# Performance work log

Hardware: AMD Instinct MI355X
Metric: run time of the kernel (lower is better)

The kernel has to match this reference:

```python
import jax, jax.numpy as jnp
import numpy as np

B, N, T, E, H, R = 8, 64, 128, 128, 8, 4
DH = E // H


def setup_inputs() -> dict:
    key = jax.random.key(0)
    ks = jax.random.split(key, 14)
    s = 1.0 / np.sqrt(E)
    return {
        "node_memory": jax.random.normal(ks[0], (B, N, T, E), jnp.float32),
        "subgraph_memory": jax.random.normal(ks[1], (B, N, T, E, R - 1), jnp.float32),
        "Wq": jax.random.normal(ks[2], (E, E), jnp.float32) * s,
        "bq": jnp.zeros((E,), jnp.float32),
        "Wk": jax.random.normal(ks[3], (E, E), jnp.float32) * s,
        "bk": jnp.zeros((E,), jnp.float32),
        "Wv": jax.random.normal(ks[4], (E, E), jnp.float32) * s,
        "bv": jnp.zeros((E,), jnp.float32),
        "in_w": jax.random.normal(ks[5], (3 * E, E), jnp.float32) * s,
        "in_b": jnp.zeros((3 * E,), jnp.float32),
        "out_w": jax.random.normal(ks[6], (E, E), jnp.float32) * s,
        "out_b": jnp.zeros((E,), jnp.float32),
        "fc_w": jax.random.normal(ks[7], (E, R * E), jnp.float32) * (1.0 / np.sqrt(R * E)),
        "fc_b": jnp.zeros((E,), jnp.float32),
    }


def reference(node_memory, subgraph_memory, Wq, bq, Wk, bk, Wv, bv,
              in_w, in_b, out_w, out_b, fc_w, fc_b):
    # combined: [B,N,T,R,E] = concat(node[...,None,:], subgraph permuted)
    combined = jnp.concatenate(
        [node_memory[..., None, :], jnp.swapaxes(subgraph_memory, -1, -2)], axis=-2)
    # outer QKV projections
    Q = jnp.einsum("bntrf,ef->bntre", combined, Wq) + bq
    K = jnp.einsum("bntrf,ef->bntre", combined, Wk) + bk
    V = jnp.einsum("bntrf,ef->bntre", combined, Wv) + bv
    # nn.MultiheadAttention in-projection
    q = jnp.einsum("bntre,fe->bntrf", Q, in_w[:E]) + in_b[:E]
    k = jnp.einsum("bntre,fe->bntrf", K, in_w[E:2 * E]) + in_b[E:2 * E]
    v = jnp.einsum("bntre,fe->bntrf", V, in_w[2 * E:]) + in_b[2 * E:]
    # split heads: [B,N,T,R,H,DH]
    q = q.reshape(B, N, T, R, H, DH) * (1.0 / np.sqrt(DH))
    k = k.reshape(B, N, T, R, H, DH)
    v = v.reshape(B, N, T, R, H, DH)
    scores = jnp.einsum("bntrhd,bntshd->bnthrs", q, k)  # [B,N,T,H,R,R]
    attn = jax.nn.softmax(scores, axis=-1)
    o = jnp.einsum("bnthrs,bntshd->bntrhd", attn, v).reshape(B, N, T, R, E)
    o = jnp.einsum("bntre,fe->bntrf", o, out_w) + out_b
    # concat the R representations and fuse
    o = o.reshape(B, N, T, R * E)
    return jnp.einsum("bntc,ec->bnte", o, fc_w) + fc_b
```

## Files before the change

kernel.cpp:

```cpp
#include <hip/hip_runtime.h>
#include <hip/hip_bf16.h>

constexpr int cE  = 128;
constexpr int cR  = 4;
constexpr int cNT = 65536;

typedef short s8v  __attribute__((ext_vector_type(8)));
typedef float f4v  __attribute__((ext_vector_type(4)));

static __device__ __forceinline__ unsigned short f2bf(float x) {
    union { float f; unsigned int u; } v; v.f = x;
    unsigned int r = v.u + 0x7fffu + ((v.u >> 16) & 1u);
    return (unsigned short)(r >> 16);
}

#define QB(x, C) __int_as_float(__builtin_amdgcn_update_dpp( \
            0, __float_as_int(x), C, 0xF, 0xF, false))

__global__ __launch_bounds__(256) void k_prep(
    const float* __restrict__ Wq, const float* __restrict__ Wk, const float* __restrict__ Wv,
    const float* __restrict__ in_w, const float* __restrict__ out_w, const float* __restrict__ fc_w,
    const float* __restrict__ bq, const float* __restrict__ bk, const float* __restrict__ bv,
    const float* __restrict__ in_b, const float* __restrict__ out_b, const float* __restrict__ fc_b,
    unsigned short* __restrict__ wqkv, unsigned short* __restrict__ meff,
    float* __restrict__ bqkv, float* __restrict__ beff)
{
    int bid = blockIdx.x;
    if (bid < 1792) {
        int gt = bid * 256 + (int)threadIdx.x;
        int o  = gt >> 2;
        int p  = gt & 3;
        float s;
        if (o < 3 * cE * cE) {
            int w   = o >> 14;
            int rem = o & (cE * cE - 1);
            int f = rem >> 7, g = rem & 127;
            const float* Wsel = (w == 0) ? Wq : ((w == 1) ? Wk : Wv);
            const float* iw = in_w + (size_t)(w * cE + f) * cE + p * 32;
            const float* wp = Wsel + (size_t)(p * 32) * cE + g;
            float s0 = 0.f, s1 = 0.f;
            #pragma unroll
            for (int e = 0; e < 32; e += 2) {
                s0 += iw[e]     * wp[(size_t)e * cE];
                s1 += iw[e + 1] * wp[(size_t)(e + 1) * cE];
            }
            s = s0 + s1;
            s += __shfl_xor(s, 1);
            s += __shfl_xor(s, 2);
            if (w == 0) s *= 0.25f;
            if (p == 0) wqkv[o] = f2bf(s);
        } else {
            int i2 = o - 3 * cE * cE;
            int e1 = i2 >> 9;
            int c  = i2 & 511;
            const float* fw = fc_w + (size_t)e1 * 512 + (c >> 7) * cE + p * 32;
            int ee = c & 127;
            const float* ow = out_w + (size_t)(p * 32) * cE + ee;
            float s0 = 0.f, s1 = 0.f;
            #pragma unroll
            for (int ff = 0; ff < 32; ff += 2) {
                s0 += fw[ff]     * ow[(size_t)ff * cE];
                s1 += fw[ff + 1] * ow[(size_t)(ff + 1) * cE];
            }
            s = s0 + s1;
            s += __shfl_xor(s, 1);
            s += __shfl_xor(s, 2);
            if (p == 0) meff[i2] = f2bf(s);
        }
    } else {
        int idx = (bid - 1792) * 256 + (int)threadIdx.x;
        if (idx < 384) {
            int w = idx >> 7, f = idx & 127;
            const float* bsel = (w == 0) ? bq : ((w == 1) ? bk : bv);
            const float* iw = in_w + (size_t)(w * cE + f) * cE;
            float s = 0.f;
            for (int e = 0; e < cE; ++e) s += iw[e] * bsel[e];
            s += in_b[w * cE + f];
            if (w == 0) s *= 0.25f;
            bqkv[idx] = s;
        } else {
            int f = idx - 384;
            float s = 0.f;
            for (int c = 0; c < 512; ++c) s += fc_w[(size_t)f * 512 + c] * out_b[c & 127];
            beff[f] = s + fc_b[f];
        }
    }
}

#define TOKB   32
#define TOKC   8
#define PITCH  136
#define OPITCH 520

__global__ __launch_bounds__(256) void k_main(
    const float* __restrict__ node, const float* __restrict__ sub,
    const unsigned short* __restrict__ wqkv,
    const unsigned short* __restrict__ meff,
    const float* __restrict__ bqkv,
    const float* __restrict__ beff,
    float* __restrict__ out)
{
    __shared__ unsigned short uAO[32 * PITCH];

    const int tid  = threadIdx.x;
    const int lane = tid & 63;
    const int wv   = tid >> 6;
    const int l15  = lane & 15;
    const int lq   = lane >> 4;
    const int ct0  = wv * 2;

    const int tokBlock = blockIdx.x * TOKB;

    for (int chunk = 0; chunk < TOKB / TOKC; ++chunk) {
        const int tokBase = tokBlock + chunk * TOKC;
        __syncthreads();

        {
            int tok = tid >> 5;
            int e4  = (tid & 31) * 4;
            float4 v = *(const float4*)(node + (size_t)(tokBase + tok) * cE + e4);
            *(ushort4*)&uAO[(tok * cR) * PITCH + e4] =
                make_ushort4(f2bf(v.x), f2bf(v.y), f2bf(v.z), f2bf(v.w));
        }
        {
            int tok = tid >> 5;
            int eg  = tid & 31;
            const float* sp = sub + (size_t)(tokBase + tok) * 384 + eg * 12;
            float4 f0 = *(const float4*)(sp + 0);
            float4 f1 = *(const float4*)(sp + 4);
            float4 f2 = *(const float4*)(sp + 8);
            int e0 = eg * 4;
            *(ushort4*)&uAO[(tok * cR + 1) * PITCH + e0] =
                make_ushort4(f2bf(f0.x), f2bf(f0.w), f2bf(f1.z), f2bf(f2.y));
            *(ushort4*)&uAO[(tok * cR + 2) * PITCH + e0] =
                make_ushort4(f2bf(f0.y), f2bf(f1.x), f2bf(f1.w), f2bf(f2.z));
            *(ushort4*)&uAO[(tok * cR + 3) * PITCH + e0] =
                make_ushort4(f2bf(f0.z), f2bf(f1.y), f2bf(f2.x), f2bf(f2.w));
        }
        __syncthreads();

        f4v qa[2][2], ka[2][2], va[2][2];
        #pragma unroll
        for (int rt = 0; rt < 2; ++rt)
            #pragma unroll
            for (int cc = 0; cc < 2; ++cc) {
                qa[rt][cc] = (f4v){0.f, 0.f, 0.f, 0.f};
                ka[rt][cc] = (f4v){0.f, 0.f, 0.f, 0.f};
                va[rt][cc] = (f4v){0.f, 0.f, 0.f, 0.f};
            }
        #pragma unroll
        for (int kc = 0; kc < 4; ++kc) {
            const int koff = kc * 32 + lq * 8;
            s8v a0 = *(const s8v*)&uAO[l15 * PITCH + koff];
            s8v a1 = *(const s8v*)&uAO[(16 + l15) * PITCH + koff];
            #pragma unroll
            for (int cc = 0; cc < 2; ++cc) {
                const size_t fo = (size_t)((ct0 + cc) * 16 + l15) * cE + koff;
                s8v wq_ = *(const s8v*)(wqkv + fo);
                s8v wk_ = *(const s8v*)(wqkv + 16384 + fo);
                s8v wv_ = *(const s8v*)(wqkv + 32768 + fo);
                qa[0][cc] = __builtin_amdgcn_mfma_f32_16x16x32_bf16(wq_, a0, qa[0][cc], 0, 0, 0);
                qa[1][cc] = __builtin_amdgcn_mfma_f32_16x16x32_bf16(wq_, a1, qa[1][cc], 0, 0, 0);
                ka[0][cc] = __builtin_amdgcn_mfma_f32_16x16x32_bf16(wk_, a0, ka[0][cc], 0, 0, 0);
                ka[1][cc] = __builtin_amdgcn_mfma_f32_16x16x32_bf16(wk_, a1, ka[1][cc], 0, 0, 0);
                va[0][cc] = __builtin_amdgcn_mfma_f32_16x16x32_bf16(wv_, a0, va[0][cc], 0, 0, 0);
                va[1][cc] = __builtin_amdgcn_mfma_f32_16x16x32_bf16(wv_, a1, va[1][cc], 0, 0, 0);
            }
        }
        #pragma unroll
        for (int cc = 0; cc < 2; ++cc) {
            const int fb = (ct0 + cc) * 16 + lq * 4;
            float4 b0 = *(const float4*)(bqkv + fb);
            float4 b1 = *(const float4*)(bqkv + cE + fb);
            float4 b2 = *(const float4*)(bqkv + 2 * cE + fb);
            #pragma unroll
            for (int rt = 0; rt < 2; ++rt) {
                qa[rt][cc][0] += b0.x; qa[rt][cc][1] += b0.y;
                qa[rt][cc][2] += b0.z; qa[rt][cc][3] += b0.w;
                ka[rt][cc][0] += b1.x; ka[rt][cc][1] += b1.y;
                ka[rt][cc][2] += b1.z; ka[rt][cc][3] += b1.w;
                va[rt][cc][0] += b2.x; va[rt][cc][1] += b2.y;
                va[rt][cc][2] += b2.z; va[rt][cc][3] += b2.w;
            }
        }

        __syncthreads();

        {
            const int r  = l15 & 3;
            const int tq = l15 >> 2;
            #pragma unroll
            for (int rt = 0; rt < 2; ++rt) {
                #pragma unroll
                for (int cc = 0; cc < 2; ++cc) {
                    f4v q = qa[rt][cc], k = ka[rt][cc], v = va[rt][cc];
                    float s0 = QB(k[0],0x00)*q[0] + QB(k[1],0x00)*q[1]
                             + QB(k[2],0x00)*q[2] + QB(k[3],0x00)*q[3];
                    float s1 = QB(k[0],0x55)*q[0] + QB(k[1],0x55)*q[1]
                             + QB(k[2],0x55)*q[2] + QB(k[3],0x55)*q[3];
                    float s2 = QB(k[0],0xAA)*q[0] + QB(k[1],0xAA)*q[1]
                             + QB(k[2],0xAA)*q[2] + QB(k[3],0xAA)*q[3];
                    float s3 = QB(k[0],0xFF)*q[0] + QB(k[1],0xFF)*q[1]
                             + QB(k[2],0xFF)*q[2] + QB(k[3],0xFF)*q[3];
                    s0 += __shfl_xor(s0, 16); s0 += __shfl_xor(s0, 32);
                    s1 += __shfl_xor(s1, 16); s1 += __shfl_xor(s1, 32);
                    s2 += __shfl_xor(s2, 16); s2 += __shfl_xor(s2, 32);
                    s3 += __shfl_xor(s3, 16); s3 += __shfl_xor(s3, 32);
                    float m = fmaxf(fmaxf(s0, s1), fmaxf(s2, s3));
                    float p0 = __expf(s0 - m), p1 = __expf(s1 - m);
                    float p2 = __expf(s2 - m), p3 = __expf(s3 - m);
                    float inv = 1.f / (p0 + p1 + p2 + p3);
                    p0 *= inv; p1 *= inv; p2 *= inv; p3 *= inv;
                    float o0 = p0*QB(v[0],0x00) + p1*QB(v[0],0x55)
                             + p2*QB(v[0],0xAA) + p3*QB(v[0],0xFF);
                    float o1 = p0*QB(v[1],0x00) + p1*QB(v[1],0x55)
                             + p2*QB(v[1],0xAA) + p3*QB(v[1],0xFF);
                    float o2 = p0*QB(v[2],0x00) + p1*QB(v[2],0x55)
                             + p2*QB(v[2],0xAA) + p3*QB(v[2],0xFF);
                    float o3 = p0*QB(v[3],0x00) + p1*QB(v[3],0x55)
                             + p2*QB(v[3],0xAA) + p3*QB(v[3],0xFF);
                    int tok = rt * 4 + tq;
                    *(ushort4*)&uAO[tok * OPITCH + r * cE + (ct0 + cc) * 16 + lq * 4] =
                        make_ushort4(f2bf(o0), f2bf(o1), f2bf(o2), f2bf(o3));
                }
            }
        }
        __syncthreads();

        {
            f4v acc[2];
            acc[0] = (f4v){0.f, 0.f, 0.f, 0.f};
            acc[1] = (f4v){0.f, 0.f, 0.f, 0.f};
            int arow = l15 & 7;
            #pragma unroll 4
            for (int kc = 0; kc < 16; ++kc) {
                int koff = kc * 32 + lq * 8;
                s8v a = *(const s8v*)&uAO[arow * OPITCH + koff];
                #pragma unroll
                for (int c = 0; c < 2; ++c) {
                    int e1 = (ct0 + c) * 16 + l15;
                    s8v b = *(const s8v*)(meff + (size_t)e1 * 512 + koff);
                    acc[c] = __builtin_amdgcn_mfma_f32_16x16x32_bf16(b, a, acc[c], 0, 0, 0);
                }
            }
            if (l15 < 8) {
                size_t tokOff = (size_t)(tokBase + l15) * cE;
                #pragma unroll
                for (int c = 0; c < 2; ++c) {
                    int col = (ct0 + c) * 16 + lq * 4;
                    float4 b4 = *(const float4*)&beff[col];
                    *(float4*)&out[tokOff + col] =
                        make_float4(acc[c][0] + b4.x, acc[c][1] + b4.y,
                                    acc[c][2] + b4.z, acc[c][3] + b4.w);
                }
            }
        }
    }
}

extern "C" void kernel_launch(void* const* d_in, const int* in_sizes, int n_in,
                              void* d_out, int out_size, void* d_ws, size_t ws_size,
                              hipStream_t stream) {
    const float* node  = (const float*)d_in[0];
    const float* sub   = (const float*)d_in[1];
    const float* Wq    = (const float*)d_in[2];
    const float* bq    = (const float*)d_in[3];
    const float* Wk    = (const float*)d_in[4];
    const float* bk    = (const float*)d_in[5];
    const float* Wv    = (const float*)d_in[6];
    const float* bv    = (const float*)d_in[7];
    const float* in_w  = (const float*)d_in[8];
    const float* in_b  = (const float*)d_in[9];
    const float* out_w = (const float*)d_in[10];
    const float* out_b = (const float*)d_in[11];
    const float* fc_w  = (const float*)d_in[12];
    const float* fc_b  = (const float*)d_in[13];

    unsigned short* ws_wqkv = (unsigned short*)d_ws;
    unsigned short* ws_meff = ws_wqkv + 3 * cE * cE;
    float* ws_bqkv = (float*)((char*)d_ws + (size_t)(3 * cE * cE + cE * cR * cE) * 2);
    float* ws_beff = ws_bqkv + 3 * cE;

    k_prep<<<dim3(1794), dim3(256), 0, stream>>>(Wq, Wk, Wv, in_w, out_w, fc_w,
                                                 bq, bk, bv, in_b, out_b, fc_b,
                                                 ws_wqkv, ws_meff, ws_bqkv, ws_beff);
    k_main<<<dim3(cNT / TOKB), dim3(256), 0, stream>>>(node, sub, ws_wqkv, ws_meff,
                                                       ws_bqkv, ws_beff, (float*)d_out);
}
```

Measured before the change: 348.6 us.

## Double-buffer shared tiles and prefetch next chunk's inputs into registers

Splits the single shared buffer into double-buffered input (sA) and attention-output (sO) tiles. The global loads for the next 8-token chunk are issued into registers before the QKV MFMAs of the current chunk, then converted and written to the other buffer after the attention step. This removes two of the per-chunk barriers and overlaps global memory latency with compute. It also adds a waves_per_eu(4) occupancy hint; the larger shared footprint and extra live registers may lower occupancy.

```diff
diff --git a/kernel.cpp b/kernel.cpp
--- a/kernel.cpp
+++ b/kernel.cpp
@@ -92,7 +92,8 @@
 #define PITCH  136
 #define OPITCH 520
 
-__global__ __launch_bounds__(256) void k_main(
+__global__ __launch_bounds__(256) __attribute__((amdgpu_waves_per_eu(4)))
+void k_main(
     const float* __restrict__ node, const float* __restrict__ sub,
     const unsigned short* __restrict__ wqkv,
     const unsigned short* __restrict__ meff,
@@ -100,7 +101,8 @@
     const float* __restrict__ beff,
     float* __restrict__ out)
 {
-    __shared__ unsigned short uAO[32 * PITCH];
+    __shared__ unsigned short sA[2][32 * PITCH];
+    __shared__ unsigned short sO[2][8 * OPITCH];
 
     const int tid  = threadIdx.x;
     const int lane = tid & 63;
@@ -110,34 +112,41 @@
     const int ct0  = wv * 2;
 
     const int tokBlock = blockIdx.x * TOKB;
+    const int stok = tid >> 5;
+    const int seg  = tid & 31;
+    const int e0   = seg * 4;
+
+    {
+        const float* np = node + (size_t)(tokBlock + stok) * cE + e0;
+        const float* sp = sub  + (size_t)(tokBlock + stok) * 384 + seg * 12;
+        float4 vn = *(const float4*)np;
+        float4 f0 = *(const float4*)(sp + 0);
+        float4 f1 = *(const float4*)(sp + 4);
+        float4 f2 = *(const float4*)(sp + 8);
+        *(ushort4*)&sA[0][(stok * cR) * PITCH + e0] =
+            make_ushort4(f2bf(vn.x), f2bf(vn.y), f2bf(vn.z), f2bf(vn.w));
+        *(ushort4*)&sA[0][(stok * cR + 1) * PITCH + e0] =
+            make_ushort4(f2bf(f0.x), f2bf(f0.w), f2bf(f1.z), f2bf(f2.y));
+        *(ushort4*)&sA[0][(stok * cR + 2) * PITCH + e0] =
+            make_ushort4(f2bf(f0.y), f2bf(f1.x), f2bf(f1.w), f2bf(f2.z));
+        *(ushort4*)&sA[0][(stok * cR + 3) * PITCH + e0] =
+            make_ushort4(f2bf(f0.z), f2bf(f1.y), f2bf(f2.x), f2bf(f2.w));
+    }
+    __syncthreads();
 
     for (int chunk = 0; chunk < TOKB / TOKC; ++chunk) {
+        const int cur = chunk & 1;
         const int tokBase = tokBlock + chunk * TOKC;
-        __syncthreads();
-
-        {
-            int tok = tid >> 5;
-            int e4  = (tid & 31) * 4;
-            float4 v = *(const float4*)(node + (size_t)(tokBase + tok) * cE + e4);
-            *(ushort4*)&uAO[(tok * cR) * PITCH + e4] =
-                make_ushort4(f2bf(v.x), f2bf(v.y), f2bf(v.z), f2bf(v.w));
-        }
-        {
-            int tok = tid >> 5;
-            int eg  = tid & 31;
-            const float* sp = sub + (size_t)(tokBase + tok) * 384 + eg * 12;
-            float4 f0 = *(const float4*)(sp + 0);
-            float4 f1 = *(const float4*)(sp + 4);
-            float4 f2 = *(const float4*)(sp + 8);
-            int e0 = eg * 4;
-            *(ushort4*)&uAO[(tok * cR + 1) * PITCH + e0] =
-                make_ushort4(f2bf(f0.x), f2bf(f0.w), f2bf(f1.z), f2bf(f2.y));
-            *(ushort4*)&uAO[(tok * cR + 2) * PITCH + e0] =
-                make_ushort4(f2bf(f0.y), f2bf(f1.x), f2bf(f1.w), f2bf(f2.z));
-            *(ushort4*)&uAO[(tok * cR + 3) * PITCH + e0] =
-                make_ushort4(f2bf(f0.z), f2bf(f1.y), f2bf(f2.x), f2bf(f2.w));
-        }
-        __syncthreads();
+
+        float4 vn, f0, f1, f2;
+        if (chunk < 3) {
+            const float* np = node + (size_t)(tokBase + TOKC + stok) * cE + e0;
+            const float* sp = sub  + (size_t)(tokBase + TOKC + stok) * 384 + seg * 12;
+            vn = *(const float4*)np;
+            f0 = *(const float4*)(sp + 0);
+            f1 = *(const float4*)(sp + 4);
+            f2 = *(const float4*)(sp + 8);
+        }
 
         f4v qa[2][2], ka[2][2], va[2][2];
         #pragma unroll
@@ -151,8 +160,8 @@
         #pragma unroll
         for (int kc = 0; kc < 4; ++kc) {
             const int koff = kc * 32 + lq * 8;
-            s8v a0 = *(const s8v*)&uAO[l15 * PITCH + koff];
-            s8v a1 = *(const s8v*)&uAO[(16 + l15) * PITCH + koff];
+            s8v a0 = *(const s8v*)&sA[cur][l15 * PITCH + koff];
+            s8v a1 = *(const s8v*)&sA[cur][(16 + l15) * PITCH + koff];
             #pragma unroll
             for (int cc = 0; cc < 2; ++cc) {
                 const size_t fo = (size_t)((ct0 + cc) * 16 + l15) * cE + koff;
@@ -183,8 +192,6 @@
                 va[rt][cc][2] += b2.z; va[rt][cc][3] += b2.w;
             }
         }
-
-        __syncthreads();
 
         {
             const int r  = l15 & 3;
@@ -220,11 +227,24 @@
                     float o3 = p0*QB(v[3],0x00) + p1*QB(v[3],0x55)
                              + p2*QB(v[3],0xAA) + p3*QB(v[3],0xFF);
                     int tok = rt * 4 + tq;
-                    *(ushort4*)&uAO[tok * OPITCH + r * cE + (ct0 + cc) * 16 + lq * 4] =
+                    *(ushort4*)&sO[cur][tok * OPITCH + r * cE + (ct0 + cc) * 16 + lq * 4] =
                         make_ushort4(f2bf(o0), f2bf(o1), f2bf(o2), f2bf(o3));
                 }
             }
         }
+
+        if (chunk < 3) {
+            unsigned short* dA = &sA[cur ^ 1][0];
+            *(ushort4*)&dA[(stok * cR) * PITCH + e0] =
+                make_ushort4(f2bf(vn.x), f2bf(vn.y), f2bf(vn.z), f2bf(vn.w));
+            *(ushort4*)&dA[(stok * cR + 1) * PITCH + e0] =
+                make_ushort4(f2bf(f0.x), f2bf(f0.w), f2bf(f1.z), f2bf(f2.y));
+            *(ushort4*)&dA[(stok * cR + 2) * PITCH + e0] =
+                make_ushort4(f2bf(f0.y), f2bf(f1.x), f2bf(f1.w), f2bf(f2.z));
+            *(ushort4*)&dA[(stok * cR + 3) * PITCH + e0] =
+                make_ushort4(f2bf(f0.z), f2bf(f1.y), f2bf(f2.x), f2bf(f2.w));
+        }
+
         __syncthreads();
 
         {
@@ -235,7 +255,7 @@
             #pragma unroll 4
             for (int kc = 0; kc < 16; ++kc) {
                 int koff = kc * 32 + lq * 8;
-                s8v a = *(const s8v*)&uAO[arow * OPITCH + koff];
+                s8v a = *(const s8v*)&sO[cur][arow * OPITCH + koff];
                 #pragma unroll
                 for (int c = 0; c < 2; ++c) {
                     int e1 = (ct0 + c) * 16 + l15;
```

Result: slower. 530.3 us (+52.1%).
